# Optimization experiments

Hardware: AMD Instinct MI355X
Metric: run time of the kernel (lower is better)

The kernel has to match this reference:

```python
import jax, jax.numpy as jnp
import numpy as np

K = 1024   # codebook size
C = 8      # codebook channels
D = K // C # per-channel code dim = 128
BETA = 0.25
B = 8192   # batch of latent vectors, each of size C*D = K


def setup_inputs() -> dict:
    key = jax.random.key(0)
    k1, k2, k3 = jax.random.split(key, 3)
    latents = jax.random.normal(k1, (B, C * D), dtype=jnp.float32)
    # nn.Embedding(K, D) init: uniform(-1/K, 1/K)
    embedding = jax.random.uniform(k2, (K, D), dtype=jnp.float32,
                                   minval=-1.0 / K, maxval=1.0 / K)
    k = jax.random.randint(k3, (C,), 0, 8, dtype=jnp.int32)
    return {"latents": latents, "embedding": embedding, "k": k}


def reference(latents, embedding, k):
    sg = jax.lax.stop_gradient
    flat = latents.reshape(-1, D)                                  # [B*C, D]
    # squared euclidean distance to every code: [B*C, K]
    dist = (jnp.sum(flat ** 2, axis=1, keepdims=True)
            + jnp.sum(embedding ** 2, axis=1)
            - 2.0 * (flat @ embedding.T))
    order = jnp.argsort(dist, axis=1).reshape(-1, C, K)            # [B, C, K]
    # per channel c, pick the k[c]-th nearest code index
    sel = jnp.take_along_axis(order, k[None, :, None], axis=2)[..., 0]  # [B, C]
    # one-hot @ embedding == plain gather of selected rows
    quantized = embedding[sel.reshape(-1)].reshape(latents.shape)  # [B, C*D]
    commitment_loss = jnp.mean((sg(quantized) - latents) ** 2)
    embedding_loss = jnp.mean((quantized - sg(latents)) ** 2)
    vq_loss = BETA * commitment_loss + embedding_loss
    # straight-through estimator
    quantized_st = latents + sg(quantized - latents)
    return quantized_st, vq_loss
```

## Files before the change

### kernel.cpp

```cpp
#include <hip/hip_runtime.h>

#define KDIM   128
#define NELEM  8388608

typedef __attribute__((ext_vector_type(4))) float f32x4;
typedef __attribute__((ext_vector_type(2))) int   int2v;

__device__ inline f32x4 mfma8(long long a, long long b, f32x4 c) {
  return __builtin_amdgcn_mfma_f32_16x16x32_fp8_fp8(a, b, c, 0, 0, 0);
}
__device__ inline void gload16(const void* g, void* l) {
  __builtin_amdgcn_global_load_lds(
      (const __attribute__((address_space(1))) unsigned*)g,
      (__attribute__((address_space(3))) unsigned*)l, 16, 0, 0);
}
__device__ inline long long pk8(float4 v0, float4 v1) {
  int lo = __builtin_amdgcn_cvt_pk_fp8_f32(v0.x, v0.y, 0, false);
  lo     = __builtin_amdgcn_cvt_pk_fp8_f32(v0.z, v0.w, lo, true);
  int hi = __builtin_amdgcn_cvt_pk_fp8_f32(v1.x, v1.y, 0, false);
  hi     = __builtin_amdgcn_cvt_pk_fp8_f32(v1.z, v1.w, hi, true);
  int2v t; t.x = lo; t.y = hi;
  return __builtin_bit_cast(long long, t);
}
__device__ inline float packk(float s, int c) {
  return __builtin_bit_cast(float,
      (__builtin_bit_cast(unsigned, s) & 0xFFFFFC00u) | (unsigned)c);
}
__device__ inline float sumsq(float4 a, float4 b) {
  return a.x*a.x + a.y*a.y + a.z*a.z + a.w*a.w + b.x*b.x + b.y*b.y + b.z*b.z + b.w*b.w;
}
__device__ inline void merge8(float (&t)[8], int msk) {
  float o[8];
#pragma unroll
  for (int p = 0; p < 8; ++p) o[p] = __shfl_xor(t[p], msk);
  float m[8];
#pragma unroll
  for (int p = 0; p < 8; ++p) m[p] = fmaxf(t[p], o[7 - p]);
#pragma unroll
  for (int s = 4; s; s >>= 1)
#pragma unroll
    for (int i = 0; i < 8; ++i)
      if (!(i & s)) {
        float x = fmaxf(m[i], m[i | s]);
        m[i | s] = fminf(m[i], m[i | s]);
        m[i] = x;
      }
#pragma unroll
  for (int p = 0; p < 8; ++p) t[p] = m[p];
}

__global__ void vq_prep(const float* __restrict__ emb, unsigned char* __restrict__ ebf8,
                        float* __restrict__ esqm, unsigned long long* __restrict__ lossAcc,
                        unsigned* __restrict__ cnt) {
  int j = blockIdx.x, d = threadIdx.x;
  float v = emb[j * KDIM + d];
  float vs = v * 1024.0f;
  int p = __builtin_amdgcn_cvt_pk_fp8_f32(vs, vs, 0, false);
  ebf8[j * KDIM + (d ^ ((j & 15) << 3))] = (unsigned char)(p & 0xFF);
  float s = v * v;
#pragma unroll
  for (int m = 1; m <= 32; m <<= 1) s += __shfl_xor(s, m);
  __shared__ float w[2];
  if ((d & 63) == 0) w[d >> 6] = s;
  __syncthreads();
  if (d == 0) esqm[j] = -512.0f * (w[0] + w[1]);
  if (j == 0 && d == 0) { lossAcc[0] = 0ULL; cnt[0] = 0u; }
}

__device__ inline void scan_codes(const unsigned char* bk0, const unsigned char* bk1,
                                  const unsigned char* bk2, const unsigned char* bk3,
                                  const float* esqmLds, int hi,
                                  long long v0, long long v1, long long v2, long long v3,
                                  float (&top)[8]) {
  int cid = hi * 4;
#pragma unroll 2
  for (int pp = 0; pp < 32; ++pp) {
    const int off = pp * 4096;
    const float* eb = esqmLds + pp * 32 + hi * 4;
    f32x4 a0 = *(const f32x4*)(eb);
    f32x4 a1 = *(const f32x4*)(eb + 16);
    f32x4 c0 = (f32x4){0.f, 0.f, 0.f, 0.f};
    f32x4 c1 = (f32x4){0.f, 0.f, 0.f, 0.f};
    a0 = mfma8(*(const long long*)(bk0 + off), v0, a0);
    a0 = mfma8(*(const long long*)(bk1 + off), v1, a0);
    c0 = mfma8(*(const long long*)(bk2 + off), v2, c0);
    c0 = mfma8(*(const long long*)(bk3 + off), v3, c0);
    a1 = mfma8(*(const long long*)(bk0 + off + 2048), v0, a1);
    a1 = mfma8(*(const long long*)(bk1 + off + 2048), v1, a1);
    c1 = mfma8(*(const long long*)(bk2 + off + 2048), v2, c1);
    c1 = mfma8(*(const long long*)(bk3 + off + 2048), v3, c1);
    a0 += c0;
    a1 += c1;
    float k0 = packk(a0[0], cid + 0),  k1 = packk(a0[1], cid + 1);
    float k2 = packk(a0[2], cid + 2),  k3 = packk(a0[3], cid + 3);
    float k4 = packk(a1[0], cid + 16), k5 = packk(a1[1], cid + 17);
    float k6 = packk(a1[2], cid + 18), k7 = packk(a1[3], cid + 19);
    float x = fmaxf(fmaxf(fmaxf(k0, k1), fmaxf(k2, k3)),
                    fmaxf(fmaxf(k4, k5), fmaxf(k6, k7)));
#pragma unroll
    for (int p = 0; p < 8; ++p) {
      float mx = fmaxf(top[p], x);
      x = fminf(top[p], x);
      top[p] = mx;
    }
    cid += 32;
  }
}

__device__ inline void write_rows(const float* __restrict__ emb, float* __restrict__ outp,
                                  int grow0, int idx, int lane) {
#pragma unroll 4
  for (int r = 0; r < 16; ++r) {
    int s2 = __shfl(idx, r);
    float2 qv = *(const float2*)(emb + (size_t)s2 * KDIM + lane * 2);
    *(float2*)(outp + (size_t)(grow0 + r) * KDIM + lane * 2) = qv;
  }
}

__global__ __launch_bounds__(1024, 4) void vq_main(
    const float* __restrict__ lat, const float* __restrict__ emb,
    const int* __restrict__ ksel, const unsigned char* __restrict__ ebf8,
    const float* __restrict__ esqm, float* __restrict__ out,
    unsigned long long* __restrict__ lossAcc, unsigned* __restrict__ cnt,
    float* __restrict__ loss) {
  __shared__ __align__(16) unsigned char smem[131072 + 4096 + 64];
  float* esqmLds = (float*)(smem + 131072);
  float* wLds    = (float*)(smem + 131072 + 4096);

  const int tid = threadIdx.x, lane = tid & 63, wid = tid >> 6;
  const int n = lane & 15, hi = lane >> 4;
  const int gR0 = blockIdx.x * 256;

  const float* rp0 = lat + (size_t)(gR0 + wid * 16 + n) * KDIM + hi * 8;
  float4 p0[4], p1[4];
#pragma unroll
  for (int ks = 0; ks < 4; ++ks) {
    p0[ks] = *(const float4*)(rp0 + ks * 32);
    p1[ks] = *(const float4*)(rp0 + ks * 32 + 4);
  }
  {
    const char* src = (const char*)ebf8 + tid * 16;
    char* dst = (char*)smem + tid * 16;
#pragma unroll
    for (int qq = 0; qq < 8; ++qq) gload16(src + qq * 16384, dst + qq * 16384);
    if (tid < 256) gload16((const char*)esqm + tid * 16, (char*)esqmLds + tid * 16);
  }
  float fsq0;
  long long b00, b01, b02, b03;
  {
    float s = 0.f;
#pragma unroll
    for (int ks = 0; ks < 4; ++ks) s += sumsq(p0[ks], p1[ks]);
    s += __shfl_xor(s, 16); s += __shfl_xor(s, 32);
    fsq0 = s;
    b00 = pk8(p0[0], p1[0]); b01 = pk8(p0[1], p1[1]);
    b02 = pk8(p0[2], p1[2]); b03 = pk8(p0[3], p1[3]);
  }
  asm volatile("s_waitcnt vmcnt(0)" ::: "memory");
  __builtin_amdgcn_s_barrier();

  const unsigned char* ab = smem + n * 128 + ((hi ^ (n & 3)) << 3);
  const int nh = n >> 2;
  const unsigned char* bk0 = ab + ((0 ^ nh) << 5);
  const unsigned char* bk1 = ab + ((1 ^ nh) << 5);
  const unsigned char* bk2 = ab + ((2 ^ nh) << 5);
  const unsigned char* bk3 = ab + ((3 ^ nh) << 5);

  const float NINF = __builtin_bit_cast(float, 0xFF800000u);
  float top0[8];
#pragma unroll
  for (int p = 0; p < 8; ++p) top0[p] = NINF;

  scan_codes(bk0, bk1, bk2, bk3, esqmLds, hi, b00, b01, b02, b03, top0);

  int kk = ksel[lane & 7];
  kk = kk < 0 ? 0 : (kk > 7 ? 7 : kk);

  merge8(top0, 16); merge8(top0, 32);
  float sel0 = top0[0];
#pragma unroll
  for (int p = 1; p < 8; ++p) sel0 = (kk == p) ? top0[p] : sel0;
  unsigned sb0 = __builtin_bit_cast(unsigned, sel0);
  int idx0 = (int)(sb0 & 1023u);
  float rl0 = fsq0 - __builtin_bit_cast(float, sb0 & 0xFFFFFC00u) * (1.0f / 512.0f);
  write_rows(emb, out, gR0 + wid * 16, idx0, lane);

  float c = (lane < 16) ? rl0 : 0.f;
#pragma unroll
  for (int m = 1; m <= 32; m <<= 1) c += __shfl_xor(c, m);
  if (lane == 0) wLds[wid] = c;
  __syncthreads();
  if (tid == 0) {
    double bs = 0.0;
#pragma unroll
    for (int w = 0; w < 16; ++w) bs += (double)wLds[w];
    long long iv = (long long)(bs * 1048576.0 + 0.5);
    atomicAdd(lossAcc, (unsigned long long)iv);
    __threadfence();
    unsigned done = atomicAdd(cnt, 1u);
    if (done == 255u) {
      unsigned long long tot = atomicAdd(lossAcc, 0ULL);
      loss[0] = (float)((double)(long long)tot * (1.25 / (1048576.0 * 8388608.0)));
    }
  }
}

extern "C" void kernel_launch(void* const* d_in, const int* in_sizes, int n_in,
                              void* d_out, int out_size, void* d_ws, size_t ws_size,
                              hipStream_t stream) {
  const float* lat = (const float*)d_in[0];
  const float* emb = (const float*)d_in[1];
  const int* ksel = (const int*)d_in[2];
  float* out = (float*)d_out;

  unsigned char* ebf8 = (unsigned char*)d_ws;
  float* esqm = (float*)((char*)d_ws + 131072);
  unsigned long long* lossAcc =
      (unsigned long long*)((char*)d_ws + 135168);
  unsigned* cnt = (unsigned*)((char*)d_ws + 135176);

  vq_prep<<<1024, 128, 0, stream>>>(emb, ebf8, esqm, lossAcc, cnt);
  vq_main<<<256, 1024, 0, stream>>>(lat, emb, ksel, ebf8, esqm, out, lossAcc, cnt,
                                    out + NELEM);
}
```

Baseline: 44.20 us.

## Split codebook scan across two blocks and merge top-8 lists in separate output kernel

The fused main kernel is split in two. A scan kernel runs 1024 blocks of 512 threads, each covering 128 rows against half of the codebook (64KB LDS), and writes per-half top-8 lists and row norms to workspace. A new output kernel merges the two lists per row, picks the k-th entry, gathers embedding rows with float4 stores, and accumulates the loss. This aims for more parallelism and occupancy during the scan, at the cost of an extra launch and a global round trip for the candidate lists.

```diff
diff --git a/kernel.cpp b/kernel.cpp
--- a/kernel.cpp
+++ b/kernel.cpp
@@ -67,28 +67,77 @@
   if (j == 0 && d == 0) { lossAcc[0] = 0ULL; cnt[0] = 0u; }
 }
 
-__device__ inline void scan_codes(const unsigned char* bk0, const unsigned char* bk1,
-                                  const unsigned char* bk2, const unsigned char* bk3,
-                                  const float* esqmLds, int hi,
-                                  long long v0, long long v1, long long v2, long long v3,
-                                  float (&top)[8]) {
-  int cid = hi * 4;
+__global__ __launch_bounds__(512, 2) void vq_scan(
+    const float* __restrict__ lat, const unsigned char* __restrict__ ebf8,
+    const float* __restrict__ esqm, float* __restrict__ fsq_g,
+    float* __restrict__ lists_g) {
+  __shared__ __align__(16) unsigned char smem[65536 + 2048];
+  float* esqmLds = (float*)(smem + 65536);
+
+  const int tid = threadIdx.x, lane = tid & 63, wid = tid >> 6;
+  const int n = lane & 15, hi = lane >> 4;
+  const int h = blockIdx.x & 1, rb = blockIdx.x >> 1;
+  const int gR0 = rb * 128;
+
+  const float* rp0 = lat + (size_t)(gR0 + wid * 16 + n) * KDIM + hi * 8;
+  float4 p0[4], p1[4];
+#pragma unroll
+  for (int ks = 0; ks < 4; ++ks) {
+    p0[ks] = *(const float4*)(rp0 + ks * 32);
+    p1[ks] = *(const float4*)(rp0 + ks * 32 + 4);
+  }
+  {
+    const char* src = (const char*)ebf8 + h * 65536 + tid * 16;
+    char* dst = (char*)smem + tid * 16;
+#pragma unroll
+    for (int qq = 0; qq < 8; ++qq) gload16(src + qq * 8192, dst + qq * 8192);
+    if (tid < 128)
+      gload16((const char*)(esqm + h * 512) + tid * 16, (char*)esqmLds + tid * 16);
+  }
+  float fsq0;
+  long long b00, b01, b02, b03;
+  {
+    float s = 0.f;
+#pragma unroll
+    for (int ks = 0; ks < 4; ++ks) s += sumsq(p0[ks], p1[ks]);
+    s += __shfl_xor(s, 16); s += __shfl_xor(s, 32);
+    fsq0 = s;
+    b00 = pk8(p0[0], p1[0]); b01 = pk8(p0[1], p1[1]);
+    b02 = pk8(p0[2], p1[2]); b03 = pk8(p0[3], p1[3]);
+  }
+  if (h == 0 && hi == 0) fsq_g[gR0 + wid * 16 + n] = fsq0;
+  asm volatile("s_waitcnt vmcnt(0)" ::: "memory");
+  __builtin_amdgcn_s_barrier();
+
+  const unsigned char* ab = smem + n * 128 + ((hi ^ (n & 3)) << 3);
+  const int nh = n >> 2;
+  const unsigned char* bk0 = ab + ((0 ^ nh) << 5);
+  const unsigned char* bk1 = ab + ((1 ^ nh) << 5);
+  const unsigned char* bk2 = ab + ((2 ^ nh) << 5);
+  const unsigned char* bk3 = ab + ((3 ^ nh) << 5);
+
+  const float NINF = __builtin_bit_cast(float, 0xFF800000u);
+  float top0[8];
+#pragma unroll
+  for (int p = 0; p < 8; ++p) top0[p] = NINF;
+
+  int cid = h * 512 + hi * 4;
 #pragma unroll 2
-  for (int pp = 0; pp < 32; ++pp) {
+  for (int pp = 0; pp < 16; ++pp) {
     const int off = pp * 4096;
     const float* eb = esqmLds + pp * 32 + hi * 4;
     f32x4 a0 = *(const f32x4*)(eb);
     f32x4 a1 = *(const f32x4*)(eb + 16);
     f32x4 c0 = (f32x4){0.f, 0.f, 0.f, 0.f};
     f32x4 c1 = (f32x4){0.f, 0.f, 0.f, 0.f};
-    a0 = mfma8(*(const long long*)(bk0 + off), v0, a0);
-    a0 = mfma8(*(const long long*)(bk1 + off), v1, a0);
-    c0 = mfma8(*(const long long*)(bk2 + off), v2, c0);
-    c0 = mfma8(*(const long long*)(bk3 + off), v3, c0);
-    a1 = mfma8(*(const long long*)(bk0 + off + 2048), v0, a1);
-    a1 = mfma8(*(const long long*)(bk1 + off + 2048), v1, a1);
-    c1 = mfma8(*(const long long*)(bk2 + off + 2048), v2, c1);
-    c1 = mfma8(*(const long long*)(bk3 + off + 2048), v3, c1);
+    a0 = mfma8(*(const long long*)(bk0 + off), b00, a0);
+    a0 = mfma8(*(const long long*)(bk1 + off), b01, a0);
+    c0 = mfma8(*(const long long*)(bk2 + off), b02, c0);
+    c0 = mfma8(*(const long long*)(bk3 + off), b03, c0);
+    a1 = mfma8(*(const long long*)(bk0 + off + 2048), b00, a1);
+    a1 = mfma8(*(const long long*)(bk1 + off + 2048), b01, a1);
+    c1 = mfma8(*(const long long*)(bk2 + off + 2048), b02, c1);
+    c1 = mfma8(*(const long long*)(bk3 + off + 2048), b03, c1);
     a0 += c0;
     a1 += c1;
     float k0 = packk(a0[0], cid + 0),  k1 = packk(a0[1], cid + 1);
@@ -99,109 +148,88 @@
                     fmaxf(fmaxf(k4, k5), fmaxf(k6, k7)));
 #pragma unroll
     for (int p = 0; p < 8; ++p) {
-      float mx = fmaxf(top[p], x);
-      x = fminf(top[p], x);
-      top[p] = mx;
+      float mx = fmaxf(top0[p], x);
+      x = fminf(top0[p], x);
+      top0[p] = mx;
     }
     cid += 32;
   }
-}
-
-__device__ inline void write_rows(const float* __restrict__ emb, float* __restrict__ outp,
-                                  int grow0, int idx, int lane) {
-#pragma unroll 4
-  for (int r = 0; r < 16; ++r) {
-    int s2 = __shfl(idx, r);
-    float2 qv = *(const float2*)(emb + (size_t)s2 * KDIM + lane * 2);
-    *(float2*)(outp + (size_t)(grow0 + r) * KDIM + lane * 2) = qv;
-  }
-}
-
-__global__ __launch_bounds__(1024, 4) void vq_main(
-    const float* __restrict__ lat, const float* __restrict__ emb,
-    const int* __restrict__ ksel, const unsigned char* __restrict__ ebf8,
-    const float* __restrict__ esqm, float* __restrict__ out,
-    unsigned long long* __restrict__ lossAcc, unsigned* __restrict__ cnt,
-    float* __restrict__ loss) {
-  __shared__ __align__(16) unsigned char smem[131072 + 4096 + 64];
-  float* esqmLds = (float*)(smem + 131072);
-  float* wLds    = (float*)(smem + 131072 + 4096);
-
-  const int tid = threadIdx.x, lane = tid & 63, wid = tid >> 6;
-  const int n = lane & 15, hi = lane >> 4;
-  const int gR0 = blockIdx.x * 256;
-
-  const float* rp0 = lat + (size_t)(gR0 + wid * 16 + n) * KDIM + hi * 8;
-  float4 p0[4], p1[4];
-#pragma unroll
-  for (int ks = 0; ks < 4; ++ks) {
-    p0[ks] = *(const float4*)(rp0 + ks * 32);
-    p1[ks] = *(const float4*)(rp0 + ks * 32 + 4);
-  }
-  {
-    const char* src = (const char*)ebf8 + tid * 16;
-    char* dst = (char*)smem + tid * 16;
-#pragma unroll
-    for (int qq = 0; qq < 8; ++qq) gload16(src + qq * 16384, dst + qq * 16384);
-    if (tid < 256) gload16((const char*)esqm + tid * 16, (char*)esqmLds + tid * 16);
-  }
-  float fsq0;
-  long long b00, b01, b02, b03;
-  {
-    float s = 0.f;
-#pragma unroll
-    for (int ks = 0; ks < 4; ++ks) s += sumsq(p0[ks], p1[ks]);
-    s += __shfl_xor(s, 16); s += __shfl_xor(s, 32);
-    fsq0 = s;
-    b00 = pk8(p0[0], p1[0]); b01 = pk8(p0[1], p1[1]);
-    b02 = pk8(p0[2], p1[2]); b03 = pk8(p0[3], p1[3]);
-  }
-  asm volatile("s_waitcnt vmcnt(0)" ::: "memory");
-  __builtin_amdgcn_s_barrier();
-
-  const unsigned char* ab = smem + n * 128 + ((hi ^ (n & 3)) << 3);
-  const int nh = n >> 2;
-  const unsigned char* bk0 = ab + ((0 ^ nh) << 5);
-  const unsigned char* bk1 = ab + ((1 ^ nh) << 5);
-  const unsigned char* bk2 = ab + ((2 ^ nh) << 5);
-  const unsigned char* bk3 = ab + ((3 ^ nh) << 5);
-
+
+  merge8(top0, 16); merge8(top0, 32);
+  if (hi == 0) {
+    float* dst = lists_g + ((size_t)(gR0 + wid * 16 + n) * 2 + h) * 8;
+    *(float4*)(dst + 0) = make_float4(top0[0], top0[1], top0[2], top0[3]);
+    *(float4*)(dst + 4) = make_float4(top0[4], top0[5], top0[6], top0[7]);
+  }
+}
+
+__global__ __launch_bounds__(256) void vq_out(
+    const float* __restrict__ emb, const int* __restrict__ ksel,
+    const float* __restrict__ lists_g, const float* __restrict__ fsq_g,
+    float* __restrict__ out, unsigned long long* __restrict__ lossAcc,
+    unsigned* __restrict__ cnt, float* __restrict__ loss) {
+  __shared__ __align__(16) float lbuf[128 * 20];
+  __shared__ int selLds[128];
+  __shared__ float wLds[2];
+
+  const int tid = threadIdx.x;
+  const int lane = tid & 63, wid = tid >> 6;
+  const int rB0 = blockIdx.x * 128;
   const float NINF = __builtin_bit_cast(float, 0xFF800000u);
-  float top0[8];
-#pragma unroll
-  for (int p = 0; p < 8; ++p) top0[p] = NINF;
-
-  scan_codes(bk0, bk1, bk2, bk3, esqmLds, hi, b00, b01, b02, b03, top0);
-
-  int kk = ksel[lane & 7];
-  kk = kk < 0 ? 0 : (kk > 7 ? 7 : kk);
-
-  merge8(top0, 16); merge8(top0, 32);
-  float sel0 = top0[0];
-#pragma unroll
-  for (int p = 1; p < 8; ++p) sel0 = (kk == p) ? top0[p] : sel0;
-  unsigned sb0 = __builtin_bit_cast(unsigned, sel0);
-  int idx0 = (int)(sb0 & 1023u);
-  float rl0 = fsq0 - __builtin_bit_cast(float, sb0 & 0xFFFFFC00u) * (1.0f / 512.0f);
-  write_rows(emb, out, gR0 + wid * 16, idx0, lane);
-
-  float c = (lane < 16) ? rl0 : 0.f;
-#pragma unroll
-  for (int m = 1; m <= 32; m <<= 1) c += __shfl_xor(c, m);
-  if (lane == 0) wLds[wid] = c;
+
+#pragma unroll
+  for (int it = 0; it < 2; ++it) {
+    int f4 = tid + it * 256;
+    int f = f4 * 4;
+    int row = f >> 4, col = f & 15;
+    float4 v = *(const float4*)(lists_g + (size_t)rB0 * 16 + f);
+    *(float4*)(&lbuf[row * 20 + col]) = v;
+  }
   __syncthreads();
+
+  float rl = 0.f;
+  if (tid < 128) {
+    const int row = rB0 + tid;
+    int kk = ksel[row & 7]; kk = kk < 0 ? 0 : (kk > 7 ? 7 : kk);
+    const float* base = lbuf + tid * 20;
+    float ha = base[0], hb = base[8];
+    int ia = 1, ib = 1;
+    float sel;
+    for (int s = 0;; ++s) {
+      sel = fmaxf(ha, hb);
+      if (s == kk) break;
+      if (sel == ha) { ha = (ia < 8) ? base[ia] : NINF; ++ia; }
+      else           { hb = (ib < 8) ? base[8 + ib] : NINF; ++ib; }
+    }
+    unsigned sb = __builtin_bit_cast(unsigned, sel);
+    selLds[tid] = (int)(sb & 1023u);
+    float val = __builtin_bit_cast(float, sb & 0xFFFFFC00u);
+    rl = fsq_g[row] - val * (1.0f / 512.0f);
+  }
+#pragma unroll
+  for (int m = 1; m <= 32; m <<= 1) rl += __shfl_xor(rl, m);
+  if (lane == 0 && wid < 2) wLds[wid] = rl;
+  __syncthreads();
+
   if (tid == 0) {
-    double bs = 0.0;
-#pragma unroll
-    for (int w = 0; w < 16; ++w) bs += (double)wLds[w];
+    double bs = (double)wLds[0] + (double)wLds[1];
     long long iv = (long long)(bs * 1048576.0 + 0.5);
     atomicAdd(lossAcc, (unsigned long long)iv);
     __threadfence();
     unsigned done = atomicAdd(cnt, 1u);
-    if (done == 255u) {
+    if (done == 511u) {
       unsigned long long tot = atomicAdd(lossAcc, 0ULL);
       loss[0] = (float)((double)(long long)tot * (1.25 / (1048576.0 * 8388608.0)));
     }
+  }
+
+#pragma unroll
+  for (int it = 0; it < 16; ++it) {
+    int i = tid + it * 256;
+    int row = i >> 5, c4 = i & 31;
+    int s2 = selLds[row];
+    float4 v = *(const float4*)(emb + (size_t)s2 * KDIM + c4 * 4);
+    *(float4*)(out + (size_t)(rB0 + row) * KDIM + c4 * 4) = v;
   }
 }
 
@@ -215,11 +243,14 @@
 
   unsigned char* ebf8 = (unsigned char*)d_ws;
   float* esqm = (float*)((char*)d_ws + 131072);
+  float* fsq_g = (float*)((char*)d_ws + 135168);
+  float* lists_g = (float*)((char*)d_ws + 397312);
   unsigned long long* lossAcc =
-      (unsigned long long*)((char*)d_ws + 135168);
-  unsigned* cnt = (unsigned*)((char*)d_ws + 135176);
+      (unsigned long long*)((char*)d_ws + 4591616);
+  unsigned* cnt = (unsigned*)((char*)d_ws + 4591624);
 
   vq_prep<<<1024, 128, 0, stream>>>(emb, ebf8, esqm, lossAcc, cnt);
-  vq_main<<<256, 1024, 0, stream>>>(lat, emb, ksel, ebf8, esqm, out, lossAcc, cnt,
-                                    out + NELEM);
-}
+  vq_scan<<<1024, 512, 0, stream>>>(lat, ebf8, esqm, fsq_g, lists_g);
+  vq_out<<<512, 256, 0, stream>>>(emb, ksel, lists_g, fsq_g, out, lossAcc, cnt,
+                                  out + NELEM);
+}
```

After: 61.65 us. +39.5%, slower.
